# Kernel optimization log

Measured on AMD Instinct MI355X. Metric: run time of the kernel, lower is better.

The kernel has to match this reference:

```python
import jax, jax.numpy as jnp
import numpy as np

N = 16384

def setup_inputs() -> dict:
    key = jax.random.key(0)
    k1, k2, k3 = jax.random.split(key, 3)
    hazard_pred = jax.random.normal(k1, (N, 1), dtype=jnp.float32)
    durations = jax.random.uniform(k2, (N,), dtype=jnp.float32)
    events = jax.random.uniform(k3, (N,), dtype=jnp.float32)
    return {"hazard_pred": hazard_pred, "durations": durations, "events": events}

def reference(hazard_pred, durations, events):
    theta = hazard_pred.reshape(-1)                      # [n]
    # risk-set mask: R[i, j] = durations[j] >= durations[i]
    R = (durations[None, :] >= durations[:, None]).astype(theta.dtype)  # [n, n]
    # sum_j exp(theta_j) * R[i, j]  -> fused masked row-sum (single GEMV)
    risk_sum = R @ jnp.exp(theta)                        # [n]
    loss_cox = -jnp.mean((theta - jnp.log(risk_sum)) * events)
    return loss_cox
```

## Files before the change

### kernel.cpp

```cpp
#include <hip/hip_runtime.h>
#include <math.h>

#define NB    2048
#define G2    32
#define TBLK  512
#define OWNB  (NB / G2)
#define CAP   1280
#define NSEG  (NB / 64)


__device__ __forceinline__ int bucket_of(float d) {
    int b = (int)(d * (float)NB);
    return min(max(b, 0), NB - 1);
}

__global__ __launch_bounds__(TBLK)
void k1_hist(const float* __restrict__ hazard,
             const float* __restrict__ durations,
             float* __restrict__ partialF,
             float* __restrict__ wsum, int* __restrict__ done, int n) {
    __shared__ float hist[NB];
    const int tid = threadIdx.x, blk = blockIdx.x;
    #pragma unroll
    for (int k = 0; k < NB / TBLK; ++k) hist[tid + k * TBLK] = 0.0f;
    __syncthreads();
    const int i = blk * TBLK + tid;
    if (i < n) atomicAdd(&hist[bucket_of(durations[i])], expf(hazard[i]));
    __syncthreads();
    #pragma unroll
    for (int k = 0; k < NB / TBLK; ++k) {
        int idx = tid + k * TBLK;
        partialF[blk * NB + idx] = hist[idx];
    }
    if (blk == 0 && tid == 0) { *wsum = 0.0f; *done = 0; }
}

__global__ __launch_bounds__(TBLK)
void k2_loss(const float* __restrict__ hazard,
             const float* __restrict__ durations,
             const float* __restrict__ events,
             const float* __restrict__ partialF, int rows,
             float* __restrict__ wsum, int* __restrict__ done,
             float* __restrict__ out, int n) {
    __shared__ float scan[NB];
    __shared__ float segSum[NSEG], segOff[NSEG];
    __shared__ float sd[CAP], se[CAP], sh[CAP];
    __shared__ int   sidx[CAP];
    __shared__ float bd[CAP], be[CAP];
    __shared__ int   lcnt[OWNB], loff[OWNB], lcur[OWNB];
    __shared__ int   nOwn;
    __shared__ float wpart[TBLK / 64];

    const int tid  = threadIdx.x, blk = blockIdx.x;
    const int base = blk * OWNB;
    const int lane = tid & 63, w = tid >> 6;

    if (tid < OWNB) lcnt[tid] = 0;
    if (tid == 0) nOwn = 0;
    __syncthreads();

    #define STASH(dd, hh, jj) {                                          \
        int lb_ = bucket_of(dd) - base;                                  \
        if (lb_ >= 0 && lb_ < OWNB) {                                    \
            int p_ = atomicAdd(&nOwn, 1);                                \
            if (p_ < CAP) {                                              \
                sd[p_] = (dd); sh[p_] = (hh); se[p_] = expf(hh);         \
                sidx[p_] = (jj); atomicAdd(&lcnt[lb_], 1);               \
            } } }
    const int n4 = n >> 2;
    const float4* dv4 = (const float4*)durations;
    const float4* hv4 = (const float4*)hazard;
    for (int q = tid; q < n4; q += TBLK) {
        float4 dv = dv4[q];
        float4 hv = hv4[q];
        int j0 = q << 2;
        STASH(dv.x, hv.x, j0);
        STASH(dv.y, hv.y, j0 + 1);
        STASH(dv.z, hv.z, j0 + 2);
        STASH(dv.w, hv.w, j0 + 3);
    }
    for (int j = (n4 << 2) + tid; j < n; j += TBLK)
        STASH(durations[j], hazard[j], j);
    #undef STASH

    #pragma unroll
    for (int r = 0; r < 4; ++r) {
        int s = w * 4 + r;
        int k = s * 64 + lane;
        int ridx = NB - 1 - k;
        float v0 = 0.0f, v1 = 0.0f, v2 = 0.0f, v3 = 0.0f;
        int g = 0;
        for (; g + 3 < rows; g += 4) {
            v0 += partialF[(g + 0) * NB + ridx];
            v1 += partialF[(g + 1) * NB + ridx];
            v2 += partialF[(g + 2) * NB + ridx];
            v3 += partialF[(g + 3) * NB + ridx];
        }
        for (; g < rows; ++g) v0 += partialF[g * NB + ridx];
        float v = (v0 + v1) + (v2 + v3);
        #pragma unroll
        for (int o = 1; o < 64; o <<= 1) {
            float y = __shfl_up(v, o, 64);
            if (lane >= o) v += y;
        }
        scan[k] = v;
        if (lane == 63) segSum[s] = v;
    }
    __syncthreads();
    if (tid < NSEG) {
        float v = segSum[tid];
        float x = v;
        #pragma unroll
        for (int o = 1; o < NSEG; o <<= 1) {
            float y = __shfl_up(x, o, 64);
            if (tid >= o) x += y;
        }
        segOff[tid] = x - v;
    }
    __syncthreads();
    #pragma unroll
    for (int r = 0; r < 4; ++r) {
        int s = w * 4 + r;
        scan[s * 64 + lane] += segOff[s];
    }
    __syncthreads();

    if (tid < 64) {
        int v = lcnt[tid];
        int x = v;
        #pragma unroll
        for (int o = 1; o < 64; o <<= 1) {
            int y = __shfl_up(x, o, 64);
            if (tid >= o) x += y;
        }
        loff[tid] = x - v;
        lcur[tid] = x - v;
    }
    __syncthreads();

    const int tot = min(nOwn, CAP);
    for (int p = tid; p < tot; p += TBLK) {
        int lb = bucket_of(sd[p]) - base;
        int q  = atomicAdd(&lcur[lb], 1);
        bd[q] = sd[p]; be[q] = se[p];
    }
    __syncthreads();

    float local = 0.0f;
    for (int p = tid; p < tot; p += TBLK) {
        float d  = sd[p];
        int   b  = bucket_of(d);
        int   lb = b - base;
        float s  = (b + 1 < NB) ? scan[NB - 2 - b] : 0.0f;
        int off = loff[lb], c = lcnt[lb];
        for (int t = 0; t < c; ++t) {
            float dj = bd[off + t];
            s += (dj >= d) ? be[off + t] : 0.0f;
        }
        local += (sh[p] - logf(s)) * events[sidx[p]];
    }

    #pragma unroll
    for (int o = 32; o > 0; o >>= 1)
        local += __shfl_down(local, o, 64);
    if ((tid & 63) == 0) wpart[tid >> 6] = local;
    __syncthreads();
    if (tid == 0) {
        float t = 0.0f;
        #pragma unroll
        for (int ww = 0; ww < TBLK / 64; ++ww) t += wpart[ww];
        atomicAdd(wsum, t);
        __threadfence();
        int ticket = atomicAdd(done, 1);
        if (ticket == (int)gridDim.x - 1)
            out[0] = -atomicAdd(wsum, 0.0f) / (float)n;
    }
}

extern "C" void kernel_launch(void* const* d_in, const int* in_sizes, int n_in,
                              void* d_out, int out_size, void* d_ws, size_t ws_size,
                              hipStream_t stream) {
    const float* hazard    = (const float*)d_in[0];
    const float* durations = (const float*)d_in[1];
    const float* events    = (const float*)d_in[2];
    float* out = (float*)d_out;
    const int n = in_sizes[1];

    char*  ws       = (char*)d_ws;
    float* partialF = (float*)(ws + 0);
    float* wsum     = (float*)(ws + 524288);
    int*   done     = (int*)  (ws + 524292);

    const int rows = (n + TBLK - 1) / TBLK;

    k1_hist<<<rows, TBLK, 0, stream>>>(hazard, durations, partialF, wsum, done, n);
    k2_loss<<<G2, TBLK, 0, stream>>>(hazard, durations, events, partialF, rows,
                                     wsum, done, out, n);
}
```

Measured before the change: 83.69 us.

## Shrink histogram partials and gather hazard/events only for owned elements

The histogram kernel now runs 1024 threads per block, each handling two elements through float2 loads. This cuts the number of per-block partial histograms from 32 to 8, so the loss kernel reads far less partial data when building its prefix scan. The loss kernel also stops streaming the full hazard array during its ownership scan. It gathers hazard, exp(hazard) and events only for the elements it owns after a barrier, which costs an extra sync and scattered gathers.

```diff
diff --git a/kernel.cpp b/kernel.cpp
--- a/kernel.cpp
+++ b/kernel.cpp
@@ -4,6 +4,7 @@
 #define NB    2048
 #define G2    32
 #define TBLK  512
+#define R1T   1024
 #define OWNB  (NB / G2)
 #define CAP   1280
 #define NSEG  (NB / 64)
@@ -14,7 +15,7 @@
     return min(max(b, 0), NB - 1);
 }
 
-__global__ __launch_bounds__(TBLK)
+__global__ __launch_bounds__(R1T)
 void k1_hist(const float* __restrict__ hazard,
              const float* __restrict__ durations,
              float* __restrict__ partialF,
@@ -22,14 +23,21 @@
     __shared__ float hist[NB];
     const int tid = threadIdx.x, blk = blockIdx.x;
     #pragma unroll
-    for (int k = 0; k < NB / TBLK; ++k) hist[tid + k * TBLK] = 0.0f;
-    __syncthreads();
-    const int i = blk * TBLK + tid;
-    if (i < n) atomicAdd(&hist[bucket_of(durations[i])], expf(hazard[i]));
-    __syncthreads();
-    #pragma unroll
-    for (int k = 0; k < NB / TBLK; ++k) {
-        int idx = tid + k * TBLK;
+    for (int k = 0; k < NB / R1T; ++k) hist[tid + k * R1T] = 0.0f;
+    __syncthreads();
+    const int i2 = blk * (R1T * 2) + tid * 2;
+    if (i2 + 1 < n) {
+        float2 dv = *(const float2*)(durations + i2);
+        float2 hv = *(const float2*)(hazard + i2);
+        atomicAdd(&hist[bucket_of(dv.x)], expf(hv.x));
+        atomicAdd(&hist[bucket_of(dv.y)], expf(hv.y));
+    } else if (i2 < n) {
+        atomicAdd(&hist[bucket_of(durations[i2])], expf(hazard[i2]));
+    }
+    __syncthreads();
+    #pragma unroll
+    for (int k = 0; k < NB / R1T; ++k) {
+        int idx = tid + k * R1T;
         partialF[blk * NB + idx] = hist[idx];
     }
     if (blk == 0 && tid == 0) { *wsum = 0.0f; *done = 0; }
@@ -44,7 +52,7 @@
              float* __restrict__ out, int n) {
     __shared__ float scan[NB];
     __shared__ float segSum[NSEG], segOff[NSEG];
-    __shared__ float sd[CAP], se[CAP], sh[CAP];
+    __shared__ float sd[CAP], se[CAP], sh[CAP], sev[CAP];
     __shared__ int   sidx[CAP];
     __shared__ float bd[CAP], be[CAP];
     __shared__ int   lcnt[OWNB], loff[OWNB], lcur[OWNB];
@@ -59,29 +67,35 @@
     if (tid == 0) nOwn = 0;
     __syncthreads();
 
-    #define STASH(dd, hh, jj) {                                          \
+    #define STASH(dd, jj) {                                              \
         int lb_ = bucket_of(dd) - base;                                  \
         if (lb_ >= 0 && lb_ < OWNB) {                                    \
             int p_ = atomicAdd(&nOwn, 1);                                \
             if (p_ < CAP) {                                              \
-                sd[p_] = (dd); sh[p_] = (hh); se[p_] = expf(hh);         \
-                sidx[p_] = (jj); atomicAdd(&lcnt[lb_], 1);               \
+                sd[p_] = (dd); sidx[p_] = (jj);                          \
+                atomicAdd(&lcnt[lb_], 1);                                \
             } } }
     const int n4 = n >> 2;
     const float4* dv4 = (const float4*)durations;
-    const float4* hv4 = (const float4*)hazard;
     for (int q = tid; q < n4; q += TBLK) {
         float4 dv = dv4[q];
-        float4 hv = hv4[q];
         int j0 = q << 2;
-        STASH(dv.x, hv.x, j0);
-        STASH(dv.y, hv.y, j0 + 1);
-        STASH(dv.z, hv.z, j0 + 2);
-        STASH(dv.w, hv.w, j0 + 3);
+        STASH(dv.x, j0);
+        STASH(dv.y, j0 + 1);
+        STASH(dv.z, j0 + 2);
+        STASH(dv.w, j0 + 3);
     }
     for (int j = (n4 << 2) + tid; j < n; j += TBLK)
-        STASH(durations[j], hazard[j], j);
+        STASH(durations[j], j);
     #undef STASH
+    __syncthreads();
+
+    const int tot = min(nOwn, CAP);
+    for (int p = tid; p < tot; p += TBLK) {
+        int j = sidx[p];
+        float h = hazard[j];
+        sh[p] = h; se[p] = expf(h); sev[p] = events[j];
+    }
 
     #pragma unroll
     for (int r = 0; r < 4; ++r) {
@@ -138,7 +152,6 @@
     }
     __syncthreads();
 
-    const int tot = min(nOwn, CAP);
     for (int p = tid; p < tot; p += TBLK) {
         int lb = bucket_of(sd[p]) - base;
         int q  = atomicAdd(&lcur[lb], 1);
@@ -157,7 +170,7 @@
             float dj = bd[off + t];
             s += (dj >= d) ? be[off + t] : 0.0f;
         }
-        local += (sh[p] - logf(s)) * events[sidx[p]];
+        local += (sh[p] - logf(s)) * sev[p];
     }
 
     #pragma unroll
@@ -191,9 +204,9 @@
     float* wsum     = (float*)(ws + 524288);
     int*   done     = (int*)  (ws + 524292);
 
-    const int rows = (n + TBLK - 1) / TBLK;
-
-    k1_hist<<<rows, TBLK, 0, stream>>>(hazard, durations, partialF, wsum, done, n);
+    const int rows = (n + (R1T * 2) - 1) / (R1T * 2);
+
+    k1_hist<<<rows, R1T, 0, stream>>>(hazard, durations, partialF, wsum, done, n);
     k2_loss<<<G2, TBLK, 0, stream>>>(hazard, durations, events, partialF, rows,
                                      wsum, done, out, n);
 }
```

Measured after the change: 75.58 us. 1.11x faster.
